# Performance work log

Hardware: AMD Instinct MI355X
Metric: run time of the kernel (lower is better)

The kernel has to match this reference:

```python
import jax, jax.numpy as jnp
import numpy as np

B, T, C = 4, 2048, 1024
QH = 4            # n_q_heads
D = C // QH       # per-head dim = 256
EPS = 1e-5


def setup_inputs() -> dict:
    key = jax.random.key(0)
    k1, k2, k3 = jax.random.split(key, 3)
    residual = jax.random.normal(k1, (B, T, C), dtype=jnp.float32)
    # scale weights ~ Xavier-ish so relu(score)^2 stays numerically sane
    w_fc = jax.random.normal(k2, (C, C), dtype=jnp.float32) * (1.0 / np.sqrt(C))
    w_proj = jax.random.normal(k3, (C, C), dtype=jnp.float32) * (1.0 / np.sqrt(C))
    ln_g = jnp.ones((C,), dtype=jnp.float32)
    ln_b = jnp.zeros((C,), dtype=jnp.float32)
    return {"residual": residual, "w_fc": w_fc, "w_proj": w_proj,
            "ln_g": ln_g, "ln_b": ln_b}


def _layernorm(x, g, b):
    mu = jnp.mean(x, axis=-1, keepdims=True)
    var = jnp.mean(jnp.square(x - mu), axis=-1, keepdims=True)
    return (x - mu) * jax.lax.rsqrt(var + EPS) * g + b


def reference(residual, w_fc, w_proj, ln_g, ln_b):
    Bx, Tx, Cx = residual.shape
    x = _layernorm(residual, ln_g, ln_b)
    # q: (B, QH, T, D)
    q = x.reshape(Bx, Tx, QH, D).transpose(0, 2, 1, 3)
    # keys: rows of w_fc chopped into 4C kv entries of dim D, shared across heads
    k = w_fc.reshape(-1, D)          # (S, D), S = 4C
    # values: columns of w_proj (i.e. w_proj^T rows) chopped the same way
    v = w_proj.T.reshape(-1, D)      # (S, D)
    scores = jnp.einsum('bhtd,sd->bhts', q, k)
    # softmax(log(relusq(score))) then *exp(lse) == plain relu(score)^2 weights
    p = jnp.square(jax.nn.relu(scores))
    out = jnp.einsum('bhts,sd->bhtd', p, v)
    out = out.transpose(0, 2, 1, 3).reshape(Bx, Tx, Cx)
    return residual + out
```

## Files before the change

### kernel.cpp

```cpp
#include <hip/hip_runtime.h>
#include <hip/hip_bf16.h>

typedef __attribute__((ext_vector_type(8))) short bf16x8;
typedef __attribute__((ext_vector_type(4))) float f32x4;

#define C_    1024
#define MROWS 32768
#define D_    256
#define S_TOT 4096
#define SCH   32
#define NCH   (S_TOT / SCH)

__device__ __forceinline__ unsigned short f2bf(float f) {
  union { float f; unsigned int u; } v; v.f = f;
  unsigned int u = v.u;
  u += 0x7fffu + ((u >> 16) & 1u);
  return (unsigned short)(u >> 16);
}

__device__ __forceinline__ void async16(const void* g, void* l) {
  __builtin_amdgcn_global_load_lds(
      (const __attribute__((address_space(1))) unsigned int*)g,
      (__attribute__((address_space(3))) unsigned int*)l, 16, 0, 0);
}

__global__ __launch_bounds__(256) void ln_kernel(const float* __restrict__ res,
                                                 const float* __restrict__ g,
                                                 const float* __restrict__ b,
                                                 unsigned short* __restrict__ xq) {
  int wave = threadIdx.x >> 6, lane = threadIdx.x & 63;
  int row = blockIdx.x * 4 + wave;
  const float* r = res + (size_t)row * C_;
  float4 x[4];
  float s = 0.f, s2 = 0.f;
  #pragma unroll
  for (int i = 0; i < 4; ++i) {
    x[i] = *(const float4*)(r + i * 256 + lane * 4);
    s  += x[i].x + x[i].y + x[i].z + x[i].w;
    s2 += x[i].x * x[i].x + x[i].y * x[i].y + x[i].z * x[i].z + x[i].w * x[i].w;
  }
  #pragma unroll
  for (int off = 32; off > 0; off >>= 1) {
    s  += __shfl_xor(s, off, 64);
    s2 += __shfl_xor(s2, off, 64);
  }
  float mu  = s * (1.0f / C_);
  float var = s2 * (1.0f / C_) - mu * mu;
  float rs  = rsqrtf(var + 1e-5f);
  #pragma unroll
  for (int i = 0; i < 4; ++i) {
    int c = i * 256 + lane * 4;
    float4 gg = *(const float4*)(g + c);
    float4 bb = *(const float4*)(b + c);
    unsigned short o[4];
    o[0] = f2bf((x[i].x - mu) * rs * gg.x + bb.x);
    o[1] = f2bf((x[i].y - mu) * rs * gg.y + bb.y);
    o[2] = f2bf((x[i].z - mu) * rs * gg.z + bb.z);
    o[3] = f2bf((x[i].w - mu) * rs * gg.w + bb.w);
    *(ushort4*)(xq + (size_t)row * C_ + c) = *(ushort4*)o;
  }
}

__global__ __launch_bounds__(256) void prep_k(const float* __restrict__ wfc,
                                              unsigned short* __restrict__ kq) {
  int t = blockIdx.x * 256 + threadIdx.x;
  int lane = t & 63;
  int sn  = (t >> 6) & 1;
  int kc  = (t >> 7) & 7;
  int sc2 = t >> 10;
  int s = sc2 * 32 + sn * 16 + (lane & 15);
  int d = kc * 32 + (lane >> 4) * 8;
  const float* src = wfc + (size_t)s * D_ + d;
  float4 a = *(const float4*)src;
  float4 b = *(const float4*)(src + 4);
  unsigned short o[8] = { f2bf(a.x), f2bf(a.y), f2bf(a.z), f2bf(a.w),
                          f2bf(b.x), f2bf(b.y), f2bf(b.z), f2bf(b.w) };
  *(uint4*)(kq + (size_t)t * 8) = *(uint4*)o;
}

__global__ __launch_bounds__(256) void prep_v(const float* __restrict__ wproj,
                                              unsigned short* __restrict__ vq) {
  __shared__ unsigned short tile[8192];
  int b = blockIdx.x;
  int tid = threadIdx.x;
  int c0 = b * 8;
  #pragma unroll
  for (int it = 0; it < 4; ++it) {
    int row = it * 256 + tid;
    const float* src = wproj + (size_t)row * C_ + c0;
    float4 a = *(const float4*)src;
    float4 bb = *(const float4*)(src + 4);
    unsigned short* dst = &tile[row * 8];
    dst[0] = f2bf(a.x);  dst[1] = f2bf(a.y);  dst[2] = f2bf(a.z);  dst[3] = f2bf(a.w);
    dst[4] = f2bf(bb.x); dst[5] = f2bf(bb.y); dst[6] = f2bf(bb.z); dst[7] = f2bf(bb.w);
  }
  __syncthreads();
  #pragma unroll
  for (int it = 0; it < 4; ++it) {
    int slot = it * 256 + tid;
    int lane = slot & 63;
    int dn   = slot >> 6;
    int d = dn * 16 + (lane & 15);
    int sl0 = (lane >> 4) * 8;
    unsigned short o[8];
    #pragma unroll
    for (int j = 0; j < 8; ++j) {
      int sl = sl0 + j;
      o[j] = tile[((sl & 3) * 256 + d) * 8 + (sl >> 2)];
    }
    *(uint4*)(vq + (size_t)b * 8192 + (size_t)slot * 8) = *(uint4*)o;
  }
}

__global__ __launch_bounds__(512, 2) void mlpmha_main(
    const unsigned short* __restrict__ xq,
    const unsigned short* __restrict__ kq,
    const unsigned short* __restrict__ vq,
    const float* __restrict__ res,
    float* __restrict__ out) {
  __shared__ unsigned short ldsK[2][8192];
  __shared__ unsigned short ldsV[8192];
  __shared__ unsigned short ldsP[128][36];

  int tid  = threadIdx.x;
  int wave = tid >> 6;
  int lane = tid & 63;
  int l16  = lane & 15;
  int quad = lane >> 4;
  int wgM  = blockIdx.x * 128;

  int mi = wave & 3, si = wave >> 2;
  int ni = wave & 3, mi2 = wave >> 2;

  bf16x8 qf[2][8];
  #pragma unroll
  for (int mt = 0; mt < 2; ++mt) {
    const unsigned short* qr =
        xq + (size_t)(wgM + mi * 32 + mt * 16 + l16) * D_ + quad * 8;
    #pragma unroll
    for (int kc = 0; kc < 8; ++kc) qf[mt][kc] = *(const bf16x8*)(qr + kc * 32);
  }

  f32x4 acc[4][4];
  #pragma unroll
  for (int i = 0; i < 4; ++i)
    #pragma unroll
    for (int j = 0; j < 4; ++j) acc[i][j] = (f32x4){0.f, 0.f, 0.f, 0.f};

  int soff = tid * 8;

  {
    const unsigned short* kg = kq + soff;
    async16(kg, &ldsK[0][soff]);
    async16(kg + 4096, &ldsK[0][soff + 4096]);
  }
  __syncthreads();

  for (int sc = 0; sc < NCH; ++sc) {
    int cur = sc & 1;

    {
      const unsigned short* vg = vq + (size_t)sc * 8192 + soff;
      async16(vg, &ldsV[soff]);
      async16(vg + 4096, &ldsV[soff + 4096]);
    }

    f32x4 sacc[2];
    sacc[0] = (f32x4){0.f, 0.f, 0.f, 0.f};
    sacc[1] = (f32x4){0.f, 0.f, 0.f, 0.f};
    #pragma unroll
    for (int kc = 0; kc < 8; ++kc) {
      bf16x8 kb = *(const bf16x8*)&ldsK[cur][(kc * 2 + si) * 512 + lane * 8];
      #pragma unroll
      for (int mt = 0; mt < 2; ++mt)
        sacc[mt] = __builtin_amdgcn_mfma_f32_16x16x32_bf16(qf[mt][kc], kb, sacc[mt], 0, 0, 0);
    }

    #pragma unroll
    for (int mt = 0; mt < 2; ++mt)
      #pragma unroll
      for (int r = 0; r < 4; ++r) {
        float v = sacc[mt][r];
        v = v > 0.f ? v * v : 0.f;
        ldsP[mi * 32 + mt * 16 + quad * 4 + r][si * 16 + l16] = f2bf(v);
      }

    __syncthreads();

    if (sc + 1 < NCH) {
      const unsigned short* kg = kq + (size_t)(sc + 1) * 8192 + soff;
      async16(kg, &ldsK[1 - cur][soff]);
      async16(kg + 4096, &ldsK[1 - cur][soff + 4096]);
    }

    {
      bf16x8 vb[4];
      #pragma unroll
      for (int dnl = 0; dnl < 4; ++dnl)
        vb[dnl] = *(const bf16x8*)&ldsV[((ni * 4 + dnl) * 64 + lane) * 8];
      #pragma unroll
      for (int mt2 = 0; mt2 < 4; ++mt2) {
        const unsigned short* pp = &ldsP[mi2 * 64 + mt2 * 16 + l16][quad * 8];
        union { ushort4 h[2]; bf16x8 v; } pu;
        pu.h[0] = *(const ushort4*)pp;
        pu.h[1] = *(const ushort4*)(pp + 4);
        bf16x8 pa = pu.v;
        #pragma unroll
        for (int dnl = 0; dnl < 4; ++dnl)
          acc[mt2][dnl] = __builtin_amdgcn_mfma_f32_16x16x32_bf16(pa, vb[dnl], acc[mt2][dnl], 0, 0, 0);
      }
    }

    __syncthreads();
  }

  #pragma unroll
  for (int mt2 = 0; mt2 < 4; ++mt2)
    #pragma unroll
    for (int r = 0; r < 4; ++r) {
      size_t row = (size_t)(wgM + mi2 * 64 + mt2 * 16 + quad * 4 + r) * D_;
      #pragma unroll
      for (int dnl = 0; dnl < 4; ++dnl) {
        size_t idx = row + ni * 64 + dnl * 16 + l16;
        out[idx] = res[idx] + acc[mt2][dnl][r];
      }
    }
}

extern "C" void kernel_launch(void* const* d_in, const int* in_sizes, int n_in,
                              void* d_out, int out_size, void* d_ws, size_t ws_size,
                              hipStream_t stream) {
  const float* res   = (const float*)d_in[0];
  const float* wfc   = (const float*)d_in[1];
  const float* wproj = (const float*)d_in[2];
  const float* g     = (const float*)d_in[3];
  const float* b     = (const float*)d_in[4];
  float* out = (float*)d_out;

  unsigned short* xq = (unsigned short*)d_ws;
  unsigned short* kq = xq + (size_t)MROWS * D_;
  unsigned short* vq = kq + (size_t)S_TOT * D_;

  ln_kernel<<<2048, 256, 0, stream>>>(res, g, b, xq);
  prep_k<<<512, 256, 0, stream>>>(wfc, kq);
  prep_v<<<128, 256, 0, stream>>>(wproj, vq);
  mlpmha_main<<<256, 512, 0, stream>>>(xq, kq, vq, res, out);
}
```

Baseline: 243.0 us.

## Fuse layernorm into main kernel and merge K/V prep kernels

Each workgroup of the main kernel now layer-normalises its own 32 residual rows into a 64 KB LDS tile and reads the Q fragments from there. This removes the separate layernorm launch and the bf16 round trip of the normalised activations through global memory. The K and V conversion kernels are merged into one launch that branches on block index. The extra LDS raises per-workgroup shared memory to roughly 113 KB, which may cut occupancy below the two workgroups per CU the launch bounds ask for. The layernorm work also now sits serially before the main loop in every workgroup.

```diff
diff --git a/kernel.cpp b/kernel.cpp
--- a/kernel.cpp
+++ b/kernel.cpp
@@ -24,103 +24,69 @@
       (__attribute__((address_space(3))) unsigned int*)l, 16, 0, 0);
 }
 
-__global__ __launch_bounds__(256) void ln_kernel(const float* __restrict__ res,
-                                                 const float* __restrict__ g,
-                                                 const float* __restrict__ b,
-                                                 unsigned short* __restrict__ xq) {
-  int wave = threadIdx.x >> 6, lane = threadIdx.x & 63;
-  int row = blockIdx.x * 4 + wave;
-  const float* r = res + (size_t)row * C_;
-  float4 x[4];
-  float s = 0.f, s2 = 0.f;
-  #pragma unroll
-  for (int i = 0; i < 4; ++i) {
-    x[i] = *(const float4*)(r + i * 256 + lane * 4);
-    s  += x[i].x + x[i].y + x[i].z + x[i].w;
-    s2 += x[i].x * x[i].x + x[i].y * x[i].y + x[i].z * x[i].z + x[i].w * x[i].w;
-  }
-  #pragma unroll
-  for (int off = 32; off > 0; off >>= 1) {
-    s  += __shfl_xor(s, off, 64);
-    s2 += __shfl_xor(s2, off, 64);
-  }
-  float mu  = s * (1.0f / C_);
-  float var = s2 * (1.0f / C_) - mu * mu;
-  float rs  = rsqrtf(var + 1e-5f);
-  #pragma unroll
-  for (int i = 0; i < 4; ++i) {
-    int c = i * 256 + lane * 4;
-    float4 gg = *(const float4*)(g + c);
-    float4 bb = *(const float4*)(b + c);
-    unsigned short o[4];
-    o[0] = f2bf((x[i].x - mu) * rs * gg.x + bb.x);
-    o[1] = f2bf((x[i].y - mu) * rs * gg.y + bb.y);
-    o[2] = f2bf((x[i].z - mu) * rs * gg.z + bb.z);
-    o[3] = f2bf((x[i].w - mu) * rs * gg.w + bb.w);
-    *(ushort4*)(xq + (size_t)row * C_ + c) = *(ushort4*)o;
-  }
-}
-
-__global__ __launch_bounds__(256) void prep_k(const float* __restrict__ wfc,
-                                              unsigned short* __restrict__ kq) {
-  int t = blockIdx.x * 256 + threadIdx.x;
-  int lane = t & 63;
-  int sn  = (t >> 6) & 1;
-  int kc  = (t >> 7) & 7;
-  int sc2 = t >> 10;
-  int s = sc2 * 32 + sn * 16 + (lane & 15);
-  int d = kc * 32 + (lane >> 4) * 8;
-  const float* src = wfc + (size_t)s * D_ + d;
-  float4 a = *(const float4*)src;
-  float4 b = *(const float4*)(src + 4);
-  unsigned short o[8] = { f2bf(a.x), f2bf(a.y), f2bf(a.z), f2bf(a.w),
-                          f2bf(b.x), f2bf(b.y), f2bf(b.z), f2bf(b.w) };
-  *(uint4*)(kq + (size_t)t * 8) = *(uint4*)o;
-}
-
-__global__ __launch_bounds__(256) void prep_v(const float* __restrict__ wproj,
-                                              unsigned short* __restrict__ vq) {
+__global__ __launch_bounds__(256) void prep_kv(const float* __restrict__ wfc,
+                                               const float* __restrict__ wproj,
+                                               unsigned short* __restrict__ kq,
+                                               unsigned short* __restrict__ vq) {
   __shared__ unsigned short tile[8192];
-  int b = blockIdx.x;
-  int tid = threadIdx.x;
-  int c0 = b * 8;
-  #pragma unroll
-  for (int it = 0; it < 4; ++it) {
-    int row = it * 256 + tid;
-    const float* src = wproj + (size_t)row * C_ + c0;
+  if (blockIdx.x < 512) {
+    int t = blockIdx.x * 256 + threadIdx.x;
+    int lane = t & 63;
+    int sn  = (t >> 6) & 1;
+    int kc  = (t >> 7) & 7;
+    int sc2 = t >> 10;
+    int s = sc2 * 32 + sn * 16 + (lane & 15);
+    int d = kc * 32 + (lane >> 4) * 8;
+    const float* src = wfc + (size_t)s * D_ + d;
     float4 a = *(const float4*)src;
-    float4 bb = *(const float4*)(src + 4);
-    unsigned short* dst = &tile[row * 8];
-    dst[0] = f2bf(a.x);  dst[1] = f2bf(a.y);  dst[2] = f2bf(a.z);  dst[3] = f2bf(a.w);
-    dst[4] = f2bf(bb.x); dst[5] = f2bf(bb.y); dst[6] = f2bf(bb.z); dst[7] = f2bf(bb.w);
-  }
-  __syncthreads();
-  #pragma unroll
-  for (int it = 0; it < 4; ++it) {
-    int slot = it * 256 + tid;
-    int lane = slot & 63;
-    int dn   = slot >> 6;
-    int d = dn * 16 + (lane & 15);
-    int sl0 = (lane >> 4) * 8;
-    unsigned short o[8];
-    #pragma unroll
-    for (int j = 0; j < 8; ++j) {
-      int sl = sl0 + j;
-      o[j] = tile[((sl & 3) * 256 + d) * 8 + (sl >> 2)];
-    }
-    *(uint4*)(vq + (size_t)b * 8192 + (size_t)slot * 8) = *(uint4*)o;
+    float4 b = *(const float4*)(src + 4);
+    unsigned short o[8] = { f2bf(a.x), f2bf(a.y), f2bf(a.z), f2bf(a.w),
+                            f2bf(b.x), f2bf(b.y), f2bf(b.z), f2bf(b.w) };
+    *(uint4*)(kq + (size_t)t * 8) = *(uint4*)o;
+  } else {
+    int b = blockIdx.x - 512;
+    int tid = threadIdx.x;
+    int c0 = b * 8;
+    #pragma unroll
+    for (int it = 0; it < 4; ++it) {
+      int row = it * 256 + tid;
+      const float* src = wproj + (size_t)row * C_ + c0;
+      float4 a = *(const float4*)src;
+      float4 bb = *(const float4*)(src + 4);
+      unsigned short* dst = &tile[row * 8];
+      dst[0] = f2bf(a.x);  dst[1] = f2bf(a.y);  dst[2] = f2bf(a.z);  dst[3] = f2bf(a.w);
+      dst[4] = f2bf(bb.x); dst[5] = f2bf(bb.y); dst[6] = f2bf(bb.z); dst[7] = f2bf(bb.w);
+    }
+    __syncthreads();
+    #pragma unroll
+    for (int it = 0; it < 4; ++it) {
+      int slot = it * 256 + tid;
+      int lane = slot & 63;
+      int dn   = slot >> 6;
+      int d = dn * 16 + (lane & 15);
+      int sl0 = (lane >> 4) * 8;
+      unsigned short o[8];
+      #pragma unroll
+      for (int j = 0; j < 8; ++j) {
+        int sl = sl0 + j;
+        o[j] = tile[((sl & 3) * 256 + d) * 8 + (sl >> 2)];
+      }
+      *(uint4*)(vq + (size_t)b * 8192 + (size_t)slot * 8) = *(uint4*)o;
+    }
   }
 }
 
 __global__ __launch_bounds__(512, 2) void mlpmha_main(
-    const unsigned short* __restrict__ xq,
     const unsigned short* __restrict__ kq,
     const unsigned short* __restrict__ vq,
     const float* __restrict__ res,
+    const float* __restrict__ g,
+    const float* __restrict__ b,
     float* __restrict__ out) {
   __shared__ unsigned short ldsK[2][8192];
   __shared__ unsigned short ldsV[8192];
   __shared__ unsigned short ldsP[128][36];
+  __shared__ unsigned short qtile[32 * 1024];
 
   int tid  = threadIdx.x;
   int wave = tid >> 6;
@@ -132,21 +98,6 @@
   int mi = wave & 3, si = wave >> 2;
   int ni = wave & 3, mi2 = wave >> 2;
 
-  bf16x8 qf[2][8];
-  #pragma unroll
-  for (int mt = 0; mt < 2; ++mt) {
-    const unsigned short* qr =
-        xq + (size_t)(wgM + mi * 32 + mt * 16 + l16) * D_ + quad * 8;
-    #pragma unroll
-    for (int kc = 0; kc < 8; ++kc) qf[mt][kc] = *(const bf16x8*)(qr + kc * 32);
-  }
-
-  f32x4 acc[4][4];
-  #pragma unroll
-  for (int i = 0; i < 4; ++i)
-    #pragma unroll
-    for (int j = 0; j < 4; ++j) acc[i][j] = (f32x4){0.f, 0.f, 0.f, 0.f};
-
   int soff = tid * 8;
 
   {
@@ -154,7 +105,59 @@
     async16(kg, &ldsK[0][soff]);
     async16(kg + 4096, &ldsK[0][soff + 4096]);
   }
+
+  {
+    int rb = blockIdx.x * 32;
+    #pragma unroll
+    for (int it = 0; it < 4; ++it) {
+      int lrow = wave * 4 + it;
+      const float* r = res + (size_t)(rb + lrow) * C_;
+      float4 x[4];
+      float s = 0.f, s2 = 0.f;
+      #pragma unroll
+      for (int i = 0; i < 4; ++i) {
+        x[i] = *(const float4*)(r + i * 256 + lane * 4);
+        s  += x[i].x + x[i].y + x[i].z + x[i].w;
+        s2 += x[i].x * x[i].x + x[i].y * x[i].y + x[i].z * x[i].z + x[i].w * x[i].w;
+      }
+      #pragma unroll
+      for (int off = 32; off > 0; off >>= 1) {
+        s  += __shfl_xor(s, off, 64);
+        s2 += __shfl_xor(s2, off, 64);
+      }
+      float mu  = s * (1.0f / C_);
+      float var = s2 * (1.0f / C_) - mu * mu;
+      float rs  = rsqrtf(var + 1e-5f);
+      #pragma unroll
+      for (int i = 0; i < 4; ++i) {
+        int c = i * 256 + lane * 4;
+        float4 gg = *(const float4*)(g + c);
+        float4 bb = *(const float4*)(b + c);
+        unsigned short o[4];
+        o[0] = f2bf((x[i].x - mu) * rs * gg.x + bb.x);
+        o[1] = f2bf((x[i].y - mu) * rs * gg.y + bb.y);
+        o[2] = f2bf((x[i].z - mu) * rs * gg.z + bb.z);
+        o[3] = f2bf((x[i].w - mu) * rs * gg.w + bb.w);
+        *(ushort4*)(&qtile[lrow * 1024 + c]) = *(ushort4*)o;
+      }
+    }
+  }
   __syncthreads();
+
+  bf16x8 qf[2][8];
+  #pragma unroll
+  for (int mt = 0; mt < 2; ++mt) {
+    int ql = mi * 32 + mt * 16 + l16;
+    const unsigned short* qr = &qtile[(ql >> 2) * 1024 + (ql & 3) * 256 + quad * 8];
+    #pragma unroll
+    for (int kc = 0; kc < 8; ++kc) qf[mt][kc] = *(const bf16x8*)(qr + kc * 32);
+  }
+
+  f32x4 acc[4][4];
+  #pragma unroll
+  for (int i = 0; i < 4; ++i)
+    #pragma unroll
+    for (int j = 0; j < 4; ++j) acc[i][j] = (f32x4){0.f, 0.f, 0.f, 0.f};
 
   for (int sc = 0; sc < NCH; ++sc) {
     int cur = sc & 1;
@@ -237,12 +240,9 @@
   const float* b     = (const float*)d_in[4];
   float* out = (float*)d_out;
 
-  unsigned short* xq = (unsigned short*)d_ws;
-  unsigned short* kq = xq + (size_t)MROWS * D_;
+  unsigned short* kq = (unsigned short*)d_ws;
   unsigned short* vq = kq + (size_t)S_TOT * D_;
 
-  ln_kernel<<<2048, 256, 0, stream>>>(res, g, b, xq);
-  prep_k<<<512, 256, 0, stream>>>(wfc, kq);
-  prep_v<<<128, 256, 0, stream>>>(wproj, vq);
-  mlpmha_main<<<256, 512, 0, stream>>>(xq, kq, vq, res, out);
-}
+  prep_kv<<<640, 256, 0, stream>>>(wfc, wproj, kq, vq);
+  mlpmha_main<<<256, 512, 0, stream>>>(kq, vq, res, g, b, out);
+}
```

Result: slower. 265.7 us (+9.4%).

## Restructure main loop into phased barriers with explicit waitcnts and MFMA priority

Applied to the files above, without the earlier changes.

Replaces the __syncthreads calls in the main loop with raw s_barrier and hand-placed s_waitcnt counters. The QK^T MFMAs are split into two halves so LDS reads of K and the async loads of V and the next K overlap with compute, and s_setprio raises wave priority around MFMA clusters. The next K chunk is now prefetched unconditionally, wrapping to chunk 0 on the last iteration, so vmcnt bookkeeping stays uniform at the cost of one redundant load. Correctness now depends on the manual waitcnt and barrier ordering being exactly right.

```diff
diff --git a/kernel.cpp b/kernel.cpp
--- a/kernel.cpp
+++ b/kernel.cpp
@@ -154,27 +154,56 @@
     async16(kg, &ldsK[0][soff]);
     async16(kg + 4096, &ldsK[0][soff + 4096]);
   }
-  __syncthreads();
+  asm volatile("s_waitcnt vmcnt(0)" ::: "memory");
+  __builtin_amdgcn_s_barrier();
 
   for (int sc = 0; sc < NCH; ++sc) {
     int cur = sc & 1;
-
+    f32x4 sacc[2];
+    sacc[0] = (f32x4){0.f, 0.f, 0.f, 0.f};
+    sacc[1] = (f32x4){0.f, 0.f, 0.f, 0.f};
+
+    bf16x8 kbr[4];
+    #pragma unroll
+    for (int kc = 0; kc < 4; ++kc)
+      kbr[kc] = *(const bf16x8*)&ldsK[cur][(kc * 2 + si) * 512 + lane * 8];
     {
       const unsigned short* vg = vq + (size_t)sc * 8192 + soff;
       async16(vg, &ldsV[soff]);
       async16(vg + 4096, &ldsV[soff + 4096]);
     }
-
-    f32x4 sacc[2];
-    sacc[0] = (f32x4){0.f, 0.f, 0.f, 0.f};
-    sacc[1] = (f32x4){0.f, 0.f, 0.f, 0.f};
-    #pragma unroll
-    for (int kc = 0; kc < 8; ++kc) {
-      bf16x8 kb = *(const bf16x8*)&ldsK[cur][(kc * 2 + si) * 512 + lane * 8];
+    __builtin_amdgcn_s_barrier();
+    asm volatile("s_waitcnt lgkmcnt(0)" ::: "memory");
+    __builtin_amdgcn_sched_barrier(0);
+    __builtin_amdgcn_s_setprio(1);
+    #pragma unroll
+    for (int kc = 0; kc < 4; ++kc)
       #pragma unroll
       for (int mt = 0; mt < 2; ++mt)
-        sacc[mt] = __builtin_amdgcn_mfma_f32_16x16x32_bf16(qf[mt][kc], kb, sacc[mt], 0, 0, 0);
-    }
+        sacc[mt] = __builtin_amdgcn_mfma_f32_16x16x32_bf16(qf[mt][kc], kbr[kc], sacc[mt], 0, 0, 0);
+    __builtin_amdgcn_s_setprio(0);
+    __builtin_amdgcn_s_barrier();
+
+    #pragma unroll
+    for (int kc = 0; kc < 4; ++kc)
+      kbr[kc] = *(const bf16x8*)&ldsK[cur][((kc + 4) * 2 + si) * 512 + lane * 8];
+    {
+      int nsc = (sc + 1 < NCH) ? sc + 1 : 0;
+      const unsigned short* kg = kq + (size_t)nsc * 8192 + soff;
+      async16(kg, &ldsK[1 - cur][soff]);
+      async16(kg + 4096, &ldsK[1 - cur][soff + 4096]);
+    }
+    __builtin_amdgcn_s_barrier();
+    asm volatile("s_waitcnt lgkmcnt(0)" ::: "memory");
+    __builtin_amdgcn_sched_barrier(0);
+    __builtin_amdgcn_s_setprio(1);
+    #pragma unroll
+    for (int kc = 0; kc < 4; ++kc)
+      #pragma unroll
+      for (int mt = 0; mt < 2; ++mt)
+        sacc[mt] = __builtin_amdgcn_mfma_f32_16x16x32_bf16(qf[mt][kc + 4], kbr[kc], sacc[mt], 0, 0, 0);
+    __builtin_amdgcn_s_setprio(0);
+    __builtin_amdgcn_s_barrier();
 
     #pragma unroll
     for (int mt = 0; mt < 2; ++mt)
@@ -184,34 +213,35 @@
         v = v > 0.f ? v * v : 0.f;
         ldsP[mi * 32 + mt * 16 + quad * 4 + r][si * 16 + l16] = f2bf(v);
       }
-
-    __syncthreads();
-
-    if (sc + 1 < NCH) {
-      const unsigned short* kg = kq + (size_t)(sc + 1) * 8192 + soff;
-      async16(kg, &ldsK[1 - cur][soff]);
-      async16(kg + 4096, &ldsK[1 - cur][soff + 4096]);
-    }
+    asm volatile("s_waitcnt vmcnt(2) lgkmcnt(0)" ::: "memory");
+    __builtin_amdgcn_s_barrier();
 
     {
       bf16x8 vb[4];
       #pragma unroll
       for (int dnl = 0; dnl < 4; ++dnl)
         vb[dnl] = *(const bf16x8*)&ldsV[((ni * 4 + dnl) * 64 + lane) * 8];
+      bf16x8 pa[4];
       #pragma unroll
       for (int mt2 = 0; mt2 < 4; ++mt2) {
         const unsigned short* pp = &ldsP[mi2 * 64 + mt2 * 16 + l16][quad * 8];
         union { ushort4 h[2]; bf16x8 v; } pu;
         pu.h[0] = *(const ushort4*)pp;
         pu.h[1] = *(const ushort4*)(pp + 4);
-        bf16x8 pa = pu.v;
+        pa[mt2] = pu.v;
+      }
+      asm volatile("s_waitcnt lgkmcnt(0)" ::: "memory");
+      __builtin_amdgcn_sched_barrier(0);
+      __builtin_amdgcn_s_setprio(1);
+      #pragma unroll
+      for (int mt2 = 0; mt2 < 4; ++mt2)
         #pragma unroll
         for (int dnl = 0; dnl < 4; ++dnl)
-          acc[mt2][dnl] = __builtin_amdgcn_mfma_f32_16x16x32_bf16(pa, vb[dnl], acc[mt2][dnl], 0, 0, 0);
-      }
-    }
-
-    __syncthreads();
+          acc[mt2][dnl] = __builtin_amdgcn_mfma_f32_16x16x32_bf16(pa[mt2], vb[dnl], acc[mt2][dnl], 0, 0, 0);
+      __builtin_amdgcn_s_setprio(0);
+    }
+    asm volatile("s_waitcnt vmcnt(0)" ::: "memory");
+    __builtin_amdgcn_s_barrier();
   }
 
   #pragma unroll
```

New measurement: 258.4 us. +6.3%, slower.
